# Kernel optimization log

Measured on AMD Instinct MI355X. Metric: run time of the kernel, lower is better.

## Reference

```python
import jax, jax.numpy as jnp
import numpy as np

WS = 11
SIGMA = 1.5
CH = 3
C1 = (0.01 * 255.0) ** 2  # 6.5025
C2 = (0.03 * 255.0) ** 2  # 58.5225


def _gauss_window():
    # 1D Gaussian -> outer product -> depthwise kernel [C, 1, ws, ws] (OIHW)
    coords = jnp.arange(WS, dtype=jnp.float32) - WS // 2
    g = jnp.exp(-coords ** 2 / (2.0 * SIGMA ** 2))
    g = g / g.sum()
    w2d = g[:, None] * g[None, :]
    return jnp.tile(w2d[None, None], (CH, 1, 1, 1))


def _dwconv(x, win):
    pad = WS // 2
    return jax.lax.conv_general_dilated(
        x, win, window_strides=(1, 1), padding=[(pad, pad), (pad, pad)],
        feature_group_count=CH,
        dimension_numbers=('NCHW', 'OIHW', 'NCHW'))


def setup_inputs() -> dict:
    key = jax.random.key(0)
    k1, k2 = jax.random.split(key)
    shape = (32, 3, 512, 512)
    img_gen = jax.random.uniform(k1, shape, jnp.float32, -1.0, 1.0)
    img_ref = jax.random.uniform(k2, shape, jnp.float32, -1.0, 1.0)
    return {"img_gen": img_gen, "img_ref": img_ref}


def reference(img_gen, img_ref):
    gen = (img_gen + 1.0) * 0.5
    ref = (img_ref + 1.0) * 0.5
    win = _gauss_window()

    mu1 = _dwconv(gen, win)
    mu2 = _dwconv(ref, win)
    mu1_sq = mu1 * mu1
    mu2_sq = mu2 * mu2
    mu1_mu2 = mu1 * mu2
    sigma1_sq = _dwconv(gen * gen, win) - mu1_sq
    sigma2_sq = _dwconv(ref * ref, win) - mu2_sq
    sigma12 = _dwconv(gen * ref, win) - mu1_mu2

    ssim_map = ((2.0 * mu1_mu2 + C1) * (2.0 * sigma12 + C2)) / (
        (mu1_sq + mu2_sq + C1) * (sigma1_sq + sigma2_sq + C2))
    return 1.0 - ssim_map.mean()
```

## Files before the change

### kernel.cpp

```cpp
#include <hip/hip_runtime.h>

typedef float v2f __attribute__((ext_vector_type(2)));

#define TX 64
#define TY 20
#define PROWS (TY + 10)
#define HSTR 67
#define IMW 512
#define IMH 512
#define NPLANES 96
#define NBX (IMW / TX)
#define NBY ((IMH + TY - 1) / TY)
#define NBLOCKS (NBX * NBY * NPLANES)

#define GW0 0.00102838f
#define GW1 0.00759877f
#define GW2 0.03600077f
#define GW3 0.10936069f
#define GW4 0.21300553f
#define GW5 0.26601172f

__device__ __forceinline__ void pkfma(v2f& acc, v2f a, v2f b) {
  asm("v_pk_fma_f32 %0, %1, %2, %0" : "+v"(acc) : "v"(a), "v"(b));
}
__device__ __forceinline__ v2f pkmul(v2f a, v2f b) {
  v2f d;
  asm("v_pk_mul_f32 %0, %1, %2" : "=v"(d) : "v"(a), "v"(b));
  return d;
}

__global__ __launch_bounds__(256, 4) void ssim_main(
    const float* __restrict__ gen, const float* __restrict__ ref,
    float* __restrict__ partial) {
  __shared__ float s_q[5][PROWS][HSTR];
  __shared__ float swsum[4];

  const float GW[11] = {GW0, GW1, GW2, GW3, GW4, GW5,
                        GW4, GW3, GW2, GW1, GW0};

  const int tid = threadIdx.x;
  const int bid = blockIdx.x;
  const int rem = bid % (NBX * NBY);
  const int plane = bid / (NBX * NBY);
  const int bx = rem % NBX;
  const int by = rem / NBX;
  const int x0 = bx * TX;
  const int y0 = by * TY;
  const float* gp = gen + (size_t)plane * (IMW * IMH);
  const float* rp = ref + (size_t)plane * (IMW * IMH);

  if (tid < PROWS * 8) {
    const int row = tid >> 3;
    const int xs = (tid & 7) * 8;
    const int gy = y0 - 5 + row;
    const int xbase = x0 + xs - 8;
    const float* grow = gp + (size_t)gy * IMW;
    const float* rrow = rp + (size_t)gy * IMW;

    v2f P[24];
    const bool interior = (bx >= 1) & (bx <= 6) & (by >= 1) & (by <= 24);
    if (interior) {
#pragma unroll
      for (int k = 0; k < 6; ++k) {
        const int c = xbase + 4 * k;
        const float4 g4 = *(const float4*)(grow + c);
        const float4 r4 = *(const float4*)(rrow + c);
        P[4 * k + 0] = (v2f){fmaf(0.5f, g4.x, 0.5f), fmaf(0.5f, r4.x, 0.5f)};
        P[4 * k + 1] = (v2f){fmaf(0.5f, g4.y, 0.5f), fmaf(0.5f, r4.y, 0.5f)};
        P[4 * k + 2] = (v2f){fmaf(0.5f, g4.z, 0.5f), fmaf(0.5f, r4.z, 0.5f)};
        P[4 * k + 3] = (v2f){fmaf(0.5f, g4.w, 0.5f), fmaf(0.5f, r4.w, 0.5f)};
      }
    } else {
      const bool rowok = (gy >= 0) && (gy < IMH);
#pragma unroll
      for (int k = 0; k < 6; ++k) {
        const int c = xbase + 4 * k;
        const bool ok = rowok && (c >= 0) && (c < IMW);
        float4 g4 = make_float4(-1.f, -1.f, -1.f, -1.f);
        float4 r4 = g4;
        if (ok) {
          g4 = *(const float4*)(grow + c);
          r4 = *(const float4*)(rrow + c);
        }
        P[4 * k + 0] = (v2f){fmaf(0.5f, g4.x, 0.5f), fmaf(0.5f, r4.x, 0.5f)};
        P[4 * k + 1] = (v2f){fmaf(0.5f, g4.y, 0.5f), fmaf(0.5f, r4.y, 0.5f)};
        P[4 * k + 2] = (v2f){fmaf(0.5f, g4.z, 0.5f), fmaf(0.5f, r4.z, 0.5f)};
        P[4 * k + 3] = (v2f){fmaf(0.5f, g4.w, 0.5f), fmaf(0.5f, r4.w, 0.5f)};
      }
    }

    v2f accP[8], accQ[8];
    float accS[8];
#pragma unroll
    for (int o = 0; o < 8; ++o) {
      accP[o] = (v2f){0.f, 0.f};
      accQ[o] = (v2f){0.f, 0.f};
      accS[o] = 0.f;
    }

#pragma unroll
    for (int p = 0; p < 18; ++p) {
      const v2f pv = P[p + 3];
      const v2f qv = pkmul(pv, pv);
      const float sv = pv.x * pv.y;
      const int olo = (p - 10 < 0) ? 0 : p - 10;
      const int ohi = (p < 7) ? p : 7;
#pragma unroll
      for (int o = olo; o <= ohi; ++o) {
        const float wt = GW[p - o];
        const v2f wv = (v2f){wt, wt};
        pkfma(accP[o], wv, pv);
        pkfma(accQ[o], wv, qv);
        accS[o] = fmaf(wt, sv, accS[o]);
      }
    }

#pragma unroll
    for (int o = 0; o < 8; ++o) s_q[0][row][xs + o] = accP[o].x;
#pragma unroll
    for (int o = 0; o < 8; ++o) s_q[1][row][xs + o] = accP[o].y;
#pragma unroll
    for (int o = 0; o < 8; ++o) s_q[2][row][xs + o] = accQ[o].x;
#pragma unroll
    for (int o = 0; o < 8; ++o) s_q[3][row][xs + o] = accQ[o].y;
#pragma unroll
    for (int o = 0; o < 8; ++o) s_q[4][row][xs + o] = accS[o];
  }
  __syncthreads();

  const int col = tid & 63;
  const int r0 = (tid >> 6) * 5;
  v2f hp[15], hq[15];
  float hs[15];
#pragma unroll
  for (int i = 0; i < 15; ++i) {
    hp[i] = (v2f){s_q[0][r0 + i][col], s_q[1][r0 + i][col]};
    hq[i] = (v2f){s_q[2][r0 + i][col], s_q[3][r0 + i][col]};
    hs[i] = s_q[4][r0 + i][col];
  }

  const float C1 = 6.5025f, C2 = 58.5225f;
  float lsum = 0.f;
#pragma unroll
  for (int o = 0; o < 5; ++o) {
    v2f mu = (v2f){0.f, 0.f};
    v2f ee = (v2f){0.f, 0.f};
    float e12 = 0.f;
#pragma unroll
    for (int t = 0; t < 11; ++t) {
      const float wt = GW[t];
      const v2f wv = (v2f){wt, wt};
      pkfma(mu, wv, hp[o + t]);
      pkfma(ee, wv, hq[o + t]);
      e12 = fmaf(wt, hs[o + t], e12);
    }
    const float mu1 = mu.x, mu2 = mu.y, e1 = ee.x, e2 = ee.y;
    const float m12 = mu1 * mu2;
    const float m1s = mu1 * mu1;
    const float m2s = mu2 * mu2;
    const float num = (2.f * m12 + C1) * (2.f * (e12 - m12) + C2);
    const float den = (m1s + m2s + C1) * ((e1 - m1s) + (e2 - m2s) + C2);
    const int y = y0 + r0 + o;
    lsum += (y < IMH) ? __fdividef(num, den) : 0.f;
  }

#pragma unroll
  for (int off = 32; off > 0; off >>= 1) lsum += __shfl_down(lsum, off, 64);
  if ((tid & 63) == 0) swsum[tid >> 6] = lsum;
  __syncthreads();
  if (tid == 0) partial[bid] = swsum[0] + swsum[1] + swsum[2] + swsum[3];
}

__global__ void ssim_reduce(const float* __restrict__ partial,
                            float* __restrict__ out) {
  const int nv = NBLOCKS / 4;
  double s = 0.0;
  for (int i = threadIdx.x; i < nv; i += 256) {
    float4 v = ((const float4*)partial)[i];
    s += (double)v.x + (double)v.y + (double)v.z + (double)v.w;
  }
#pragma unroll
  for (int off = 32; off > 0; off >>= 1) s += __shfl_down(s, off, 64);
  __shared__ double sd[4];
  if ((threadIdx.x & 63) == 0) sd[threadIdx.x >> 6] = s;
  __syncthreads();
  if (threadIdx.x == 0) {
    double npix = (double)NPLANES * (double)IMW * (double)IMH;
    out[0] = (float)(1.0 - (sd[0] + sd[1] + sd[2] + sd[3]) / npix);
  }
}

extern "C" void kernel_launch(void* const* d_in, const int* in_sizes, int n_in,
                              void* d_out, int out_size, void* d_ws, size_t ws_size,
                              hipStream_t stream) {
  (void)in_sizes; (void)n_in; (void)out_size; (void)ws_size;
  const float* gen = (const float*)d_in[0];
  const float* ref = (const float*)d_in[1];
  float* partial = (float*)d_ws;
  ssim_main<<<NBLOCKS, 256, 0, stream>>>(gen, ref, partial);
  ssim_reduce<<<1, 256, 0, stream>>>(partial, (float*)d_out);
}
```

Measured before the change: 296.1 us.

## Stream column strips through ring buffer to eliminate vertical halo recompute

Each block now processes a full 64-column strip down the whole image. It keeps horizontally blurred rows in a 30-slot shared-memory ring buffer, so only 20 new rows are blurred per chunk instead of 30. This removes the redundant halo loads and horizontal blur work. In exchange the grid shrinks to 768 blocks with long sequential loops and two barriers per chunk, which lowers parallelism and latency hiding. Partial sums switch to double precision.

```diff
diff --git a/kernel.cpp b/kernel.cpp
--- a/kernel.cpp
+++ b/kernel.cpp
@@ -4,14 +4,15 @@
 
 #define TX 64
 #define TY 20
-#define PROWS (TY + 10)
-#define HSTR 67
+#define WIN 30
+#define RING 30
+#define HSTR 65
 #define IMW 512
 #define IMH 512
 #define NPLANES 96
 #define NBX (IMW / TX)
-#define NBY ((IMH + TY - 1) / TY)
-#define NBLOCKS (NBX * NBY * NPLANES)
+#define NCHUNK ((IMH + TY - 1) / TY)
+#define NBLOCKS (NBX * NPLANES)
 
 #define GW0 0.00102838f
 #define GW1 0.00759877f
@@ -29,163 +30,189 @@
   return d;
 }
 
+__device__ __forceinline__ void hblur(
+    const float* __restrict__ gp, const float* __restrict__ rp,
+    float* __restrict__ sq, int x0, bool interior_x,
+    int nrows, int gy0, int slot0, int tid) {
+  if (tid >= nrows * 8) return;
+  const float GW[11] = {GW0, GW1, GW2, GW3, GW4, GW5,
+                        GW4, GW3, GW2, GW1, GW0};
+  const int r = tid >> 3;
+  const int xs = (tid & 7) * 8;
+  const int gy = gy0 + r;
+  int slot = slot0 + r;
+  if (slot >= RING) slot -= RING;
+  const int xbase = x0 + xs - 8;
+  const float* grow = gp + (size_t)gy * IMW;
+  const float* rrow = rp + (size_t)gy * IMW;
+
+  v2f P[24];
+  const bool rowok = (gy >= 0) & (gy < IMH);
+  if (interior_x & rowok) {
+#pragma unroll
+    for (int k = 0; k < 6; ++k) {
+      const int c = xbase + 4 * k;
+      const float4 g4 = *(const float4*)(grow + c);
+      const float4 r4 = *(const float4*)(rrow + c);
+      P[4 * k + 0] = (v2f){fmaf(0.5f, g4.x, 0.5f), fmaf(0.5f, r4.x, 0.5f)};
+      P[4 * k + 1] = (v2f){fmaf(0.5f, g4.y, 0.5f), fmaf(0.5f, r4.y, 0.5f)};
+      P[4 * k + 2] = (v2f){fmaf(0.5f, g4.z, 0.5f), fmaf(0.5f, r4.z, 0.5f)};
+      P[4 * k + 3] = (v2f){fmaf(0.5f, g4.w, 0.5f), fmaf(0.5f, r4.w, 0.5f)};
+    }
+  } else {
+#pragma unroll
+    for (int k = 0; k < 6; ++k) {
+      const int c = xbase + 4 * k;
+      const bool ok = rowok && (c >= 0) && (c < IMW);
+      float4 g4 = make_float4(-1.f, -1.f, -1.f, -1.f);
+      float4 r4 = g4;
+      if (ok) {
+        g4 = *(const float4*)(grow + c);
+        r4 = *(const float4*)(rrow + c);
+      }
+      P[4 * k + 0] = (v2f){fmaf(0.5f, g4.x, 0.5f), fmaf(0.5f, r4.x, 0.5f)};
+      P[4 * k + 1] = (v2f){fmaf(0.5f, g4.y, 0.5f), fmaf(0.5f, r4.y, 0.5f)};
+      P[4 * k + 2] = (v2f){fmaf(0.5f, g4.z, 0.5f), fmaf(0.5f, r4.z, 0.5f)};
+      P[4 * k + 3] = (v2f){fmaf(0.5f, g4.w, 0.5f), fmaf(0.5f, r4.w, 0.5f)};
+    }
+  }
+
+  v2f accP[8], accQ[8];
+  float accS[8];
+#pragma unroll
+  for (int o = 0; o < 8; ++o) {
+    accP[o] = (v2f){0.f, 0.f};
+    accQ[o] = (v2f){0.f, 0.f};
+    accS[o] = 0.f;
+  }
+
+#pragma unroll
+  for (int p = 0; p < 18; ++p) {
+    const v2f pv = P[p + 3];
+    const v2f qv = pkmul(pv, pv);
+    const float sv = pv.x * pv.y;
+    const int olo = (p - 10 < 0) ? 0 : p - 10;
+    const int ohi = (p < 7) ? p : 7;
+#pragma unroll
+    for (int o = olo; o <= ohi; ++o) {
+      const float wt = GW[p - o];
+      const v2f wv = (v2f){wt, wt};
+      pkfma(accP[o], wv, pv);
+      pkfma(accQ[o], wv, qv);
+      accS[o] = fmaf(wt, sv, accS[o]);
+    }
+  }
+
+  float* dst = sq + slot * (5 * HSTR) + xs;
+#pragma unroll
+  for (int o = 0; o < 8; ++o) dst[0 * HSTR + o] = accP[o].x;
+#pragma unroll
+  for (int o = 0; o < 8; ++o) dst[1 * HSTR + o] = accP[o].y;
+#pragma unroll
+  for (int o = 0; o < 8; ++o) dst[2 * HSTR + o] = accQ[o].x;
+#pragma unroll
+  for (int o = 0; o < 8; ++o) dst[3 * HSTR + o] = accQ[o].y;
+#pragma unroll
+  for (int o = 0; o < 8; ++o) dst[4 * HSTR + o] = accS[o];
+}
+
 __global__ __launch_bounds__(256, 4) void ssim_main(
     const float* __restrict__ gen, const float* __restrict__ ref,
-    float* __restrict__ partial) {
-  __shared__ float s_q[5][PROWS][HSTR];
-  __shared__ float swsum[4];
+    double* __restrict__ partial) {
+  __shared__ float s_q[RING][5][HSTR];
+  __shared__ double swsum[4];
 
   const float GW[11] = {GW0, GW1, GW2, GW3, GW4, GW5,
                         GW4, GW3, GW2, GW1, GW0};
 
   const int tid = threadIdx.x;
   const int bid = blockIdx.x;
-  const int rem = bid % (NBX * NBY);
-  const int plane = bid / (NBX * NBY);
-  const int bx = rem % NBX;
-  const int by = rem / NBX;
+  const int bx = bid & (NBX - 1);
+  const int plane = bid >> 3;
   const int x0 = bx * TX;
-  const int y0 = by * TY;
   const float* gp = gen + (size_t)plane * (IMW * IMH);
   const float* rp = ref + (size_t)plane * (IMW * IMH);
-
-  if (tid < PROWS * 8) {
-    const int row = tid >> 3;
-    const int xs = (tid & 7) * 8;
-    const int gy = y0 - 5 + row;
-    const int xbase = x0 + xs - 8;
-    const float* grow = gp + (size_t)gy * IMW;
-    const float* rrow = rp + (size_t)gy * IMW;
-
-    v2f P[24];
-    const bool interior = (bx >= 1) & (bx <= 6) & (by >= 1) & (by <= 24);
-    if (interior) {
-#pragma unroll
-      for (int k = 0; k < 6; ++k) {
-        const int c = xbase + 4 * k;
-        const float4 g4 = *(const float4*)(grow + c);
-        const float4 r4 = *(const float4*)(rrow + c);
-        P[4 * k + 0] = (v2f){fmaf(0.5f, g4.x, 0.5f), fmaf(0.5f, r4.x, 0.5f)};
-        P[4 * k + 1] = (v2f){fmaf(0.5f, g4.y, 0.5f), fmaf(0.5f, r4.y, 0.5f)};
-        P[4 * k + 2] = (v2f){fmaf(0.5f, g4.z, 0.5f), fmaf(0.5f, r4.z, 0.5f)};
-        P[4 * k + 3] = (v2f){fmaf(0.5f, g4.w, 0.5f), fmaf(0.5f, r4.w, 0.5f)};
+  const bool interior_x = (bx >= 1) & (bx <= NBX - 2);
+
+  const int col = tid & 63;
+  const int r0 = __builtin_amdgcn_readfirstlane((tid >> 6) * 5);
+
+  double acc = 0.0;
+
+  hblur(gp, rp, &s_q[0][0][0], x0, interior_x, WIN, -5, 0, tid);
+
+  int base = 0;
+  for (int c = 0; c < NCHUNK; ++c) {
+    if (c > 0) {
+      int s0 = base + 10;
+      if (s0 >= RING) s0 -= RING;
+      hblur(gp, rp, &s_q[0][0][0], x0, interior_x, TY, TY * c + 5, s0, tid);
+    }
+    __syncthreads();
+
+    int b2 = base + r0;
+    if (b2 >= RING) b2 -= RING;
+    v2f hp[15], hq[15];
+    float hs[15];
+#pragma unroll
+    for (int i = 0; i < 15; ++i) {
+      int slot = b2 + i;
+      if (slot >= RING) slot -= RING;
+      const float* rowp = &s_q[slot][0][col];
+      hp[i] = (v2f){rowp[0 * HSTR], rowp[1 * HSTR]};
+      hq[i] = (v2f){rowp[2 * HSTR], rowp[3 * HSTR]};
+      hs[i] = rowp[4 * HSTR];
+    }
+
+    const float C1 = 6.5025f, C2 = 58.5225f;
+    float lsum = 0.f;
+#pragma unroll
+    for (int o = 0; o < 5; ++o) {
+      v2f mu = (v2f){0.f, 0.f};
+      v2f ee = (v2f){0.f, 0.f};
+      float e12 = 0.f;
+#pragma unroll
+      for (int t = 0; t < 11; ++t) {
+        const float wt = GW[t];
+        const v2f wv = (v2f){wt, wt};
+        pkfma(mu, wv, hp[o + t]);
+        pkfma(ee, wv, hq[o + t]);
+        e12 = fmaf(wt, hs[o + t], e12);
       }
-    } else {
-      const bool rowok = (gy >= 0) && (gy < IMH);
-#pragma unroll
-      for (int k = 0; k < 6; ++k) {
-        const int c = xbase + 4 * k;
-        const bool ok = rowok && (c >= 0) && (c < IMW);
-        float4 g4 = make_float4(-1.f, -1.f, -1.f, -1.f);
-        float4 r4 = g4;
-        if (ok) {
-          g4 = *(const float4*)(grow + c);
-          r4 = *(const float4*)(rrow + c);
-        }
-        P[4 * k + 0] = (v2f){fmaf(0.5f, g4.x, 0.5f), fmaf(0.5f, r4.x, 0.5f)};
-        P[4 * k + 1] = (v2f){fmaf(0.5f, g4.y, 0.5f), fmaf(0.5f, r4.y, 0.5f)};
-        P[4 * k + 2] = (v2f){fmaf(0.5f, g4.z, 0.5f), fmaf(0.5f, r4.z, 0.5f)};
-        P[4 * k + 3] = (v2f){fmaf(0.5f, g4.w, 0.5f), fmaf(0.5f, r4.w, 0.5f)};
-      }
-    }
-
-    v2f accP[8], accQ[8];
-    float accS[8];
-#pragma unroll
-    for (int o = 0; o < 8; ++o) {
-      accP[o] = (v2f){0.f, 0.f};
-      accQ[o] = (v2f){0.f, 0.f};
-      accS[o] = 0.f;
-    }
-
-#pragma unroll
-    for (int p = 0; p < 18; ++p) {
-      const v2f pv = P[p + 3];
-      const v2f qv = pkmul(pv, pv);
-      const float sv = pv.x * pv.y;
-      const int olo = (p - 10 < 0) ? 0 : p - 10;
-      const int ohi = (p < 7) ? p : 7;
-#pragma unroll
-      for (int o = olo; o <= ohi; ++o) {
-        const float wt = GW[p - o];
-        const v2f wv = (v2f){wt, wt};
-        pkfma(accP[o], wv, pv);
-        pkfma(accQ[o], wv, qv);
-        accS[o] = fmaf(wt, sv, accS[o]);
-      }
-    }
-
-#pragma unroll
-    for (int o = 0; o < 8; ++o) s_q[0][row][xs + o] = accP[o].x;
-#pragma unroll
-    for (int o = 0; o < 8; ++o) s_q[1][row][xs + o] = accP[o].y;
-#pragma unroll
-    for (int o = 0; o < 8; ++o) s_q[2][row][xs + o] = accQ[o].x;
-#pragma unroll
-    for (int o = 0; o < 8; ++o) s_q[3][row][xs + o] = accQ[o].y;
-#pragma unroll
-    for (int o = 0; o < 8; ++o) s_q[4][row][xs + o] = accS[o];
-  }
-  __syncthreads();
-
-  const int col = tid & 63;
-  const int r0 = (tid >> 6) * 5;
-  v2f hp[15], hq[15];
-  float hs[15];
-#pragma unroll
-  for (int i = 0; i < 15; ++i) {
-    hp[i] = (v2f){s_q[0][r0 + i][col], s_q[1][r0 + i][col]};
-    hq[i] = (v2f){s_q[2][r0 + i][col], s_q[3][r0 + i][col]};
-    hs[i] = s_q[4][r0 + i][col];
-  }
-
-  const float C1 = 6.5025f, C2 = 58.5225f;
-  float lsum = 0.f;
-#pragma unroll
-  for (int o = 0; o < 5; ++o) {
-    v2f mu = (v2f){0.f, 0.f};
-    v2f ee = (v2f){0.f, 0.f};
-    float e12 = 0.f;
-#pragma unroll
-    for (int t = 0; t < 11; ++t) {
-      const float wt = GW[t];
-      const v2f wv = (v2f){wt, wt};
-      pkfma(mu, wv, hp[o + t]);
-      pkfma(ee, wv, hq[o + t]);
-      e12 = fmaf(wt, hs[o + t], e12);
-    }
-    const float mu1 = mu.x, mu2 = mu.y, e1 = ee.x, e2 = ee.y;
-    const float m12 = mu1 * mu2;
-    const float m1s = mu1 * mu1;
-    const float m2s = mu2 * mu2;
-    const float num = (2.f * m12 + C1) * (2.f * (e12 - m12) + C2);
-    const float den = (m1s + m2s + C1) * ((e1 - m1s) + (e2 - m2s) + C2);
-    const int y = y0 + r0 + o;
-    lsum += (y < IMH) ? __fdividef(num, den) : 0.f;
-  }
-
-#pragma unroll
-  for (int off = 32; off > 0; off >>= 1) lsum += __shfl_down(lsum, off, 64);
-  if ((tid & 63) == 0) swsum[tid >> 6] = lsum;
+      const float mu1 = mu.x, mu2 = mu.y, e1 = ee.x, e2 = ee.y;
+      const float m12 = mu1 * mu2;
+      const float m1s = mu1 * mu1;
+      const float m2s = mu2 * mu2;
+      const float num = (2.f * m12 + C1) * (2.f * (e12 - m12) + C2);
+      const float den = (m1s + m2s + C1) * ((e1 - m1s) + (e2 - m2s) + C2);
+      const int y = TY * c + r0 + o;
+      lsum += (y < IMH) ? __fdividef(num, den) : 0.f;
+    }
+    acc += (double)lsum;
+
+    __syncthreads();
+    base += TY;
+    if (base >= RING) base -= RING;
+  }
+
+#pragma unroll
+  for (int off = 32; off > 0; off >>= 1) acc += __shfl_down(acc, off, 64);
+  if ((tid & 63) == 0) swsum[tid >> 6] = acc;
   __syncthreads();
   if (tid == 0) partial[bid] = swsum[0] + swsum[1] + swsum[2] + swsum[3];
 }
 
-__global__ void ssim_reduce(const float* __restrict__ partial,
+__global__ void ssim_reduce(const double* __restrict__ partial,
                             float* __restrict__ out) {
-  const int nv = NBLOCKS / 4;
-  double s = 0.0;
-  for (int i = threadIdx.x; i < nv; i += 256) {
-    float4 v = ((const float4*)partial)[i];
-    s += (double)v.x + (double)v.y + (double)v.z + (double)v.w;
-  }
+  const int tid = threadIdx.x;
+  double s = partial[tid] + partial[tid + 256] + partial[tid + 512];
 #pragma unroll
   for (int off = 32; off > 0; off >>= 1) s += __shfl_down(s, off, 64);
   __shared__ double sd[4];
-  if ((threadIdx.x & 63) == 0) sd[threadIdx.x >> 6] = s;
+  if ((tid & 63) == 0) sd[tid >> 6] = s;
   __syncthreads();
-  if (threadIdx.x == 0) {
-    double npix = (double)NPLANES * (double)IMW * (double)IMH;
+  if (tid == 0) {
+    const double npix = (double)NPLANES * (double)IMW * (double)IMH;
     out[0] = (float)(1.0 - (sd[0] + sd[1] + sd[2] + sd[3]) / npix);
   }
 }
@@ -196,7 +223,7 @@
   (void)in_sizes; (void)n_in; (void)out_size; (void)ws_size;
   const float* gen = (const float*)d_in[0];
   const float* ref = (const float*)d_in[1];
-  float* partial = (float*)d_ws;
+  double* partial = (double*)d_ws;
   ssim_main<<<NBLOCKS, 256, 0, stream>>>(gen, ref, partial);
   ssim_reduce<<<1, 256, 0, stream>>>(partial, (float*)d_out);
 }
```

New measurement: 314.2 us. 1.06x slower.
